# Optimization experiments

Measured on AMD Instinct MI355X. Metric: run time of the kernel, lower is better.

The kernel has to match this reference:

```python
import jax, jax.numpy as jnp
import numpy as np

N, IN_SZ, OUT_SZ = 8192, 512, 64

def setup_inputs() -> dict:
    key = jax.random.key(0)
    ks = jax.random.split(key, 7)
    s_in = 1.0 / np.sqrt(IN_SZ)
    inp = {
        "input": jax.random.normal(ks[0], (N, IN_SZ), dtype=jnp.float32),
        "Wq": jax.random.uniform(ks[1], (OUT_SZ, IN_SZ), jnp.float32, -s_in, s_in),
        "bq": jax.random.uniform(ks[2], (OUT_SZ,), jnp.float32, -s_in, s_in),
        "Wk": jax.random.uniform(ks[3], (OUT_SZ, IN_SZ), jnp.float32, -s_in, s_in),
        "bk": jax.random.uniform(ks[4], (OUT_SZ,), jnp.float32, -s_in, s_in),
        "Wv": jax.random.uniform(ks[5], (OUT_SZ, IN_SZ), jnp.float32, -s_in, s_in),
        "bv": jax.random.uniform(ks[6], (OUT_SZ,), jnp.float32, -s_in, s_in),
    }
    return inp

def reference(input, Wq, bq, Wk, bk, Wv, bv):
    # torch nn.Linear: x @ W.T + b
    q = input @ Wq.T + bq  # [N, out]
    k = input @ Wk.T + bk  # [N, out]
    v = input @ Wv.T + bv  # [N, out]
    # NOTE: original module has NO 1/sqrt(d) scaling.
    scores = jax.nn.softmax(q @ k.T, axis=-1)  # [N, N]
    return scores @ v  # [N, out]
```

## Files before the change

kernel.cpp:

```cpp
#include <hip/hip_runtime.h>
#include <math.h>

#define SA_N   8192
#define SA_IN  512
#define SA_D   64
#define G_SPL  16
#define LOG2E  1.44269504f

typedef short s16x8 __attribute__((ext_vector_type(8)));
typedef float f32x16 __attribute__((ext_vector_type(16)));

#define MFMA32(A, B, C) __builtin_amdgcn_mfma_f32_32x32x16_bf16((A), (B), (C), 0, 0, 0)

static __device__ __forceinline__ unsigned short f2bf_rn(float x) {
    unsigned int u = __float_as_uint(x);
    unsigned int r = (u + 0x7FFFu + ((u >> 16) & 1u)) >> 16;
    return (unsigned short)r;
}

static __device__ __forceinline__ void trunc_split(float f, unsigned short* hi, unsigned short* lo) {
    unsigned int u = __float_as_uint(f);
    *hi = (unsigned short)(u >> 16);
    float lf = f - __uint_as_float(u & 0xFFFF0000u);
    *lo = (unsigned short)(__float_as_uint(lf) >> 16);
}

static __device__ __forceinline__ unsigned int pack_hi16(unsigned int u0, unsigned int u1) {
    return __builtin_amdgcn_perm(u1, u0, 0x07060302u);
}

static __device__ __forceinline__ void split8(const float4 a, const float4 b, s16x8* xh, s16x8* xl) {
    union { unsigned int u[4]; s16x8 v; } H, L;
    const float f[8] = {a.x, a.y, a.z, a.w, b.x, b.y, b.z, b.w};
#pragma unroll
    for (int p = 0; p < 4; ++p) {
        const unsigned int u0 = __float_as_uint(f[2 * p]);
        const unsigned int u1 = __float_as_uint(f[2 * p + 1]);
        H.u[p] = pack_hi16(u0, u1);
        const float l0 = f[2 * p]     - __uint_as_float(u0 & 0xFFFF0000u);
        const float l1 = f[2 * p + 1] - __uint_as_float(u1 & 0xFFFF0000u);
        L.u[p] = pack_hi16(__float_as_uint(l0), __float_as_uint(l1));
    }
    *xh = H.v; *xl = L.v;
}

static __device__ __forceinline__ s16x8 pack_rn8(const float4 a, const float4 b) {
    union { unsigned int u[4]; s16x8 v; } P;
    const float f[8] = {a.x, a.y, a.z, a.w, b.x, b.y, b.z, b.w};
#pragma unroll
    for (int p = 0; p < 4; ++p)
        P.u[p] = (unsigned int)f2bf_rn(f[2 * p]) | ((unsigned int)f2bf_rn(f[2 * p + 1]) << 16);
    return P.v;
}

__global__ __launch_bounds__(256, 2) void qkv_kernel(
    const float* __restrict__ in,
    const float* __restrict__ Wq, const float* __restrict__ bq,
    const float* __restrict__ Wk, const float* __restrict__ bk,
    const float* __restrict__ Wv, const float* __restrict__ bv,
    unsigned short* __restrict__ Qhi, unsigned short* __restrict__ Qlo,
    unsigned short* __restrict__ KhiF, unsigned short* __restrict__ VF)
{
    __shared__ float cbuf[2][4][64][20];
    __shared__ __align__(16) unsigned short stage[4096];
    const int t    = threadIdx.x;
    const int w    = t >> 6;
    const int lane = t & 63;
    const int h    = lane >> 5;
    const int q32  = lane & 31;
    const int mat  = blockIdx.x >> 8;
    const int jt   = blockIdx.x & 255;
    const int rows0 = jt * 32;

    const float* W = (mat == 0) ? Wq : (mat == 1 ? Wk : Wv);
    const float* B = (mat == 0) ? bq : (mat == 1 ? bk : bv);

    f32x16 accA[2] = {};
    f32x16 accB[2] = {};

#pragma unroll 2
    for (int ksl = 0; ksl < 8; ++ksl) {
        const int ks = (w << 3) + ksl;
        const float* xp = in + (size_t)(rows0 + q32) * SA_IN + ks * 16 + h * 8;
        const float4 xa = *(const float4*)xp;
        const float4 xb = *(const float4*)(xp + 4);
        s16x8 xh, xl;
        split8(xa, xb, &xh, &xl);
#pragma unroll
        for (int mt = 0; mt < 2; ++mt) {
            const float* wp = W + (size_t)(mt * 32 + q32) * SA_IN + ks * 16 + h * 8;
            const float4 wa = *(const float4*)wp;
            const float4 wb = *(const float4*)(wp + 4);
            if (mat < 2) {
                s16x8 ah, al;
                split8(wa, wb, &ah, &al);
                accA[mt] = MFMA32(ah, xh, accA[mt]);
                accB[mt] = MFMA32(ah, xl, accB[mt]);
                accA[mt] = MFMA32(al, xh, accA[mt]);
            } else {
                const s16x8 ah = pack_rn8(wa, wb);
                accA[mt] = MFMA32(ah, xh, accA[mt]);
            }
        }
    }

#pragma unroll
    for (int mt = 0; mt < 2; ++mt) {
        f32x16 tot = accA[mt];
        if (mat < 2) {
#pragma unroll
            for (int r = 0; r < 16; ++r) tot[r] += accB[mt][r];
        }
#pragma unroll
        for (int rg = 0; rg < 4; ++rg) {
            float4 vv = { tot[4 * rg + 0], tot[4 * rg + 1],
                          tot[4 * rg + 2], tot[4 * rg + 3] };
            *(float4*)&cbuf[mt][w][lane][4 * rg] = vv;
        }
    }
    __syncthreads();
    if (w < 2) {
        const int mt = w;
        float c[16];
#pragma unroll
        for (int rg = 0; rg < 4; ++rg) {
            const float4 s0 = *(const float4*)&cbuf[mt][0][lane][4 * rg];
            const float4 s1 = *(const float4*)&cbuf[mt][1][lane][4 * rg];
            const float4 s2 = *(const float4*)&cbuf[mt][2][lane][4 * rg];
            const float4 s3 = *(const float4*)&cbuf[mt][3][lane][4 * rg];
            c[4 * rg + 0] = (s0.x + s1.x) + (s2.x + s3.x);
            c[4 * rg + 1] = (s0.y + s1.y) + (s2.y + s3.y);
            c[4 * rg + 2] = (s0.z + s1.z) + (s2.z + s3.z);
            c[4 * rg + 3] = (s0.w + s1.w) + (s2.w + s3.w);
        }
#pragma unroll
        for (int r = 0; r < 16; ++r) {
            const int o = mt * 32 + (r & 3) + 8 * (r >> 2) + 4 * h;
            float val = c[r] + B[o];
            if (mat == 0) {
                val *= LOG2E;
                unsigned short hi, lo;
                trunc_split(val, &hi, &lo);
                stage[q32 * 64 + o]        = hi;
                stage[2048 + q32 * 64 + o] = lo;
            } else if (mat == 1) {
                const int kl_ = ((o >> 4) * 64 + ((o >> 3) & 1) * 32 + q32) * 8 + (o & 7);
                stage[kl_] = f2bf_rn(val);
            } else {
                const int hp = (q32 >> 2) & 1;
                const int ip = (q32 & 3) + ((q32 >> 3) & 1) * 4;
                const int vl_ = ((o >> 5) * 2 + (q32 >> 4)) * 512
                              + hp * 256 + (o & 31) * 8 + ip;
                stage[vl_] = f2bf_rn(val);
            }
        }
    }
    __syncthreads();

    {
        const uint4* st4 = (const uint4*)stage;
        if (mat == 0) {
            for (int i = t; i < 512; i += 256) {
                unsigned short* dst = ((i < 256) ? Qhi : Qlo) + (size_t)rows0 * 64 + (i & 255) * 8;
                *(uint4*)dst = st4[i];
            }
        } else if (mat == 1) {
            if (t < 256) *(uint4*)(KhiF + (size_t)jt * 2048 + t * 8) = st4[t];
        } else {
            *(uint4*)(VF + (size_t)jt * 2048 + t * 8) = st4[t];
        }
    }
}

__global__ __launch_bounds__(512, 2) void attn_kernel(
    const unsigned short* __restrict__ Qhi, const unsigned short* __restrict__ Qlo,
    const unsigned short* __restrict__ KhiF, const unsigned short* __restrict__ VF,
    unsigned short* __restrict__ Opart, float* __restrict__ Lpart)
{
    __shared__ __align__(16) unsigned short kbuf[2][2][2048];
    const int t    = threadIdx.x;
    const int w    = t >> 6;
    const int lane = t & 63;
    const int h    = lane >> 5;
    const int q32  = lane & 31;
    const int qb   = blockIdx.x >> 4;
    const int g    = blockIdx.x & 15;
    const int q0   = (qb * 8 + w) * 32;
    const int jt0  = g * 16;

    const int half = t >> 8;
    const int ti   = t & 255;

    s16x8 qh[4], ql[4];
#pragma unroll
    for (int s = 0; s < 4; ++s) {
        const size_t off = (size_t)(q0 + q32) * 64 + s * 16 + h * 8;
        qh[s] = *reinterpret_cast<const s16x8*>(Qhi + off);
        ql[s] = *reinterpret_cast<const s16x8*>(Qlo + off);
    }

    const unsigned short* SRC = half ? VF : KhiF;

    {
        const uint4 a = *(const uint4*)(SRC + (size_t)jt0 * 2048 + ti * 8);
        *(uint4*)&kbuf[0][half][ti * 8] = a;
    }
    __syncthreads();

    f32x16 O0 = {}, O1 = {};
    float lsum = 0.f;

    for (int it = 0; it < 16; ++it) {
        const int p = it & 1;

        uint4 na;
        if (it < 15) {
            na = *(const uint4*)(SRC + (size_t)(jt0 + it + 1) * 2048 + ti * 8);
        }

        s16x8 kh[4], vv[4];
#pragma unroll
        for (int s = 0; s < 4; ++s) {
            kh[s] = *(const s16x8*)&kbuf[p][0][(s * 64 + lane) * 8];
            vv[s] = *(const s16x8*)&kbuf[p][1][(s * 64 + lane) * 8];
        }

        f32x16 Sa = {}, Sb = {};
        __builtin_amdgcn_s_setprio(1);
#pragma unroll
        for (int s = 0; s < 4; ++s) {
            Sa = MFMA32(kh[s], qh[s], Sa);
            Sb = MFMA32(kh[s], ql[s], Sb);
        }
        __builtin_amdgcn_s_setprio(0);

        float e[16];
#pragma unroll
        for (int r = 0; r < 16; ++r) e[r] = __builtin_amdgcn_exp2f(Sa[r] + Sb[r]);
        lsum += (((e[0] + e[1]) + (e[2] + e[3])) + ((e[4] + e[5]) + (e[6] + e[7])))
              + (((e[8] + e[9]) + (e[10] + e[11])) + ((e[12] + e[13]) + (e[14] + e[15])));

        union { unsigned int u[4]; s16x8 v; } P0, P1;
#pragma unroll
        for (int j2 = 0; j2 < 4; ++j2) {
            P0.u[j2] = pack_hi16(__float_as_uint(e[2 * j2]),     __float_as_uint(e[2 * j2 + 1]));
            P1.u[j2] = pack_hi16(__float_as_uint(e[8 + 2 * j2]), __float_as_uint(e[8 + 2 * j2 + 1]));
        }

        __builtin_amdgcn_s_setprio(1);
        O0 = MFMA32(vv[0], P0.v, O0);
        O0 = MFMA32(vv[1], P1.v, O0);
        O1 = MFMA32(vv[2], P0.v, O1);
        O1 = MFMA32(vv[3], P1.v, O1);
        __builtin_amdgcn_s_setprio(0);

        if (it < 15) {
            *(uint4*)&kbuf[1 - p][half][ti * 8] = na;
        }
        __syncthreads();
    }

    lsum += __shfl_xor(lsum, 32, 64);

    const size_t qg = (size_t)g * SA_N + q0 + q32;
#pragma unroll
    for (int rg = 0; rg < 4; ++rg) {
        const int d0 = 8 * rg + 4 * h;
        uint2 s0, s1;
        s0.x = (unsigned int)f2bf_rn(O0[4 * rg + 0]) | ((unsigned int)f2bf_rn(O0[4 * rg + 1]) << 16);
        s0.y = (unsigned int)f2bf_rn(O0[4 * rg + 2]) | ((unsigned int)f2bf_rn(O0[4 * rg + 3]) << 16);
        s1.x = (unsigned int)f2bf_rn(O1[4 * rg + 0]) | ((unsigned int)f2bf_rn(O1[4 * rg + 1]) << 16);
        s1.y = (unsigned int)f2bf_rn(O1[4 * rg + 2]) | ((unsigned int)f2bf_rn(O1[4 * rg + 3]) << 16);
        *(uint2*)(Opart + qg * 64 + d0)      = s0;
        *(uint2*)(Opart + qg * 64 + d0 + 32) = s1;
    }
    if (h == 0) Lpart[qg] = lsum;
}

__global__ __launch_bounds__(256) void combine_kernel(
    const unsigned short* __restrict__ Opart, const float* __restrict__ Lpart,
    float* __restrict__ out)
{
    const int tid = blockIdx.x * 256 + threadIdx.x;
    const int q  = tid >> 5;
    const int dp = tid & 31;
    const unsigned int* OP = (const unsigned int*)Opart;
    float s0 = 0.f, s1 = 0.f, lt = 0.f;
#pragma unroll
    for (int g = 0; g < G_SPL; ++g) {
        const unsigned int v = OP[((size_t)g * SA_N + q) * 32 + dp];
        s0 += __uint_as_float(v << 16);
        s1 += __uint_as_float(v & 0xFFFF0000u);
        lt += Lpart[(size_t)g * SA_N + q];
    }
    float2 r = { s0 / lt, s1 / lt };
    *(float2*)&out[(size_t)q * 64 + dp * 2] = r;
}

extern "C" void kernel_launch(void* const* d_in, const int* in_sizes, int n_in,
                              void* d_out, int out_size, void* d_ws, size_t ws_size,
                              hipStream_t stream) {
    const float* input = (const float*)d_in[0];
    const float* Wq    = (const float*)d_in[1];
    const float* bq    = (const float*)d_in[2];
    const float* Wk    = (const float*)d_in[3];
    const float* bk    = (const float*)d_in[4];
    const float* Wv    = (const float*)d_in[5];
    const float* bv    = (const float*)d_in[6];
    float* out = (float*)d_out;

    const size_t SEG = (size_t)SA_N * 64;
    unsigned short* Qhi  = (unsigned short*)d_ws;
    unsigned short* Qlo  = Qhi  + SEG;
    unsigned short* KhiF = Qlo  + SEG;
    unsigned short* VF   = KhiF + SEG;
    unsigned short* Opart = VF  + SEG;
    float*          Lpart = (float*)(Opart + (size_t)G_SPL * SA_N * 64);

    qkv_kernel<<<768, 256, 0, stream>>>(input, Wq, bq, Wk, bk, Wv, bv,
                                        Qhi, Qlo, KhiF, VF);
    attn_kernel<<<32 * G_SPL, 512, 0, stream>>>(Qhi, Qlo, KhiF, VF, Opart, Lpart);
    combine_kernel<<<1024, 256, 0, stream>>>(Opart, Lpart, out);
}
```

Before: 126.2 us.

## Process two 32-row query tiles per wave to reuse K/V tiles

Each wave now handles 64 query rows (two 32-row tiles) instead of 32, so every K/V tile staged in shared memory is reused for twice as many queries. The grid is halved to 256 blocks and launch bounds drop to one block per SIMD slot to make room for the extra accumulators and Q registers. This cuts K/V global loads and LDS reads per query. The cost is higher register pressure, fewer blocks than CUs on a 256-CU part, and less latency hiding.

```diff
diff --git a/kernel.cpp b/kernel.cpp
--- a/kernel.cpp
+++ b/kernel.cpp
@@ -172,7 +172,7 @@
     }
 }
 
-__global__ __launch_bounds__(512, 2) void attn_kernel(
+__global__ __launch_bounds__(512, 1) void attn_kernel(
     const unsigned short* __restrict__ Qhi, const unsigned short* __restrict__ Qlo,
     const unsigned short* __restrict__ KhiF, const unsigned short* __restrict__ VF,
     unsigned short* __restrict__ Opart, float* __restrict__ Lpart)
@@ -185,18 +185,21 @@
     const int q32  = lane & 31;
     const int qb   = blockIdx.x >> 4;
     const int g    = blockIdx.x & 15;
-    const int q0   = (qb * 8 + w) * 32;
+    const int q0   = qb * 512 + w * 64;
     const int jt0  = g * 16;
 
     const int half = t >> 8;
     const int ti   = t & 255;
 
-    s16x8 qh[4], ql[4];
+    s16x8 qh0[4], ql0[4], qh1[4], ql1[4];
 #pragma unroll
     for (int s = 0; s < 4; ++s) {
-        const size_t off = (size_t)(q0 + q32) * 64 + s * 16 + h * 8;
-        qh[s] = *reinterpret_cast<const s16x8*>(Qhi + off);
-        ql[s] = *reinterpret_cast<const s16x8*>(Qlo + off);
+        const size_t off0 = (size_t)(q0 + q32) * 64 + s * 16 + h * 8;
+        const size_t off1 = (size_t)(q0 + 32 + q32) * 64 + s * 16 + h * 8;
+        qh0[s] = *reinterpret_cast<const s16x8*>(Qhi + off0);
+        ql0[s] = *reinterpret_cast<const s16x8*>(Qlo + off0);
+        qh1[s] = *reinterpret_cast<const s16x8*>(Qhi + off1);
+        ql1[s] = *reinterpret_cast<const s16x8*>(Qlo + off1);
     }
 
     const unsigned short* SRC = half ? VF : KhiF;
@@ -207,8 +210,8 @@
     }
     __syncthreads();
 
-    f32x16 O0 = {}, O1 = {};
-    float lsum = 0.f;
+    f32x16 O00 = {}, O01 = {}, O10 = {}, O11 = {};
+    float ls0 = 0.f, ls1 = 0.f;
 
     for (int it = 0; it < 16; ++it) {
         const int p = it & 1;
@@ -225,34 +228,67 @@
             vv[s] = *(const s16x8*)&kbuf[p][1][(s * 64 + lane) * 8];
         }
 
-        f32x16 Sa = {}, Sb = {};
-        __builtin_amdgcn_s_setprio(1);
-#pragma unroll
-        for (int s = 0; s < 4; ++s) {
-            Sa = MFMA32(kh[s], qh[s], Sa);
-            Sb = MFMA32(kh[s], ql[s], Sb);
-        }
-        __builtin_amdgcn_s_setprio(0);
-
-        float e[16];
-#pragma unroll
-        for (int r = 0; r < 16; ++r) e[r] = __builtin_amdgcn_exp2f(Sa[r] + Sb[r]);
-        lsum += (((e[0] + e[1]) + (e[2] + e[3])) + ((e[4] + e[5]) + (e[6] + e[7])))
-              + (((e[8] + e[9]) + (e[10] + e[11])) + ((e[12] + e[13]) + (e[14] + e[15])));
-
-        union { unsigned int u[4]; s16x8 v; } P0, P1;
-#pragma unroll
-        for (int j2 = 0; j2 < 4; ++j2) {
-            P0.u[j2] = pack_hi16(__float_as_uint(e[2 * j2]),     __float_as_uint(e[2 * j2 + 1]));
-            P1.u[j2] = pack_hi16(__float_as_uint(e[8 + 2 * j2]), __float_as_uint(e[8 + 2 * j2 + 1]));
-        }
-
-        __builtin_amdgcn_s_setprio(1);
-        O0 = MFMA32(vv[0], P0.v, O0);
-        O0 = MFMA32(vv[1], P1.v, O0);
-        O1 = MFMA32(vv[2], P0.v, O1);
-        O1 = MFMA32(vv[3], P1.v, O1);
-        __builtin_amdgcn_s_setprio(0);
+        {
+            f32x16 Sa = {}, Sb = {};
+            __builtin_amdgcn_s_setprio(1);
+#pragma unroll
+            for (int s = 0; s < 4; ++s) {
+                Sa = MFMA32(kh[s], qh0[s], Sa);
+                Sb = MFMA32(kh[s], ql0[s], Sb);
+            }
+            __builtin_amdgcn_s_setprio(0);
+
+            float e[16];
+#pragma unroll
+            for (int r = 0; r < 16; ++r) e[r] = __builtin_amdgcn_exp2f(Sa[r] + Sb[r]);
+            ls0 += (((e[0] + e[1]) + (e[2] + e[3])) + ((e[4] + e[5]) + (e[6] + e[7])))
+                 + (((e[8] + e[9]) + (e[10] + e[11])) + ((e[12] + e[13]) + (e[14] + e[15])));
+
+            union { unsigned int u[4]; s16x8 v; } P0, P1;
+#pragma unroll
+            for (int j2 = 0; j2 < 4; ++j2) {
+                P0.u[j2] = pack_hi16(__float_as_uint(e[2 * j2]),     __float_as_uint(e[2 * j2 + 1]));
+                P1.u[j2] = pack_hi16(__float_as_uint(e[8 + 2 * j2]), __float_as_uint(e[8 + 2 * j2 + 1]));
+            }
+
+            __builtin_amdgcn_s_setprio(1);
+            O00 = MFMA32(vv[0], P0.v, O00);
+            O00 = MFMA32(vv[1], P1.v, O00);
+            O01 = MFMA32(vv[2], P0.v, O01);
+            O01 = MFMA32(vv[3], P1.v, O01);
+            __builtin_amdgcn_s_setprio(0);
+        }
+
+        {
+            f32x16 Sa = {}, Sb = {};
+            __builtin_amdgcn_s_setprio(1);
+#pragma unroll
+            for (int s = 0; s < 4; ++s) {
+                Sa = MFMA32(kh[s], qh1[s], Sa);
+                Sb = MFMA32(kh[s], ql1[s], Sb);
+            }
+            __builtin_amdgcn_s_setprio(0);
+
+            float e[16];
+#pragma unroll
+            for (int r = 0; r < 16; ++r) e[r] = __builtin_amdgcn_exp2f(Sa[r] + Sb[r]);
+            ls1 += (((e[0] + e[1]) + (e[2] + e[3])) + ((e[4] + e[5]) + (e[6] + e[7])))
+                 + (((e[8] + e[9]) + (e[10] + e[11])) + ((e[12] + e[13]) + (e[14] + e[15])));
+
+            union { unsigned int u[4]; s16x8 v; } P0, P1;
+#pragma unroll
+            for (int j2 = 0; j2 < 4; ++j2) {
+                P0.u[j2] = pack_hi16(__float_as_uint(e[2 * j2]),     __float_as_uint(e[2 * j2 + 1]));
+                P1.u[j2] = pack_hi16(__float_as_uint(e[8 + 2 * j2]), __float_as_uint(e[8 + 2 * j2 + 1]));
+            }
+
+            __builtin_amdgcn_s_setprio(1);
+            O10 = MFMA32(vv[0], P0.v, O10);
+            O10 = MFMA32(vv[1], P1.v, O10);
+            O11 = MFMA32(vv[2], P0.v, O11);
+            O11 = MFMA32(vv[3], P1.v, O11);
+            __builtin_amdgcn_s_setprio(0);
+        }
 
         if (it < 15) {
             *(uint4*)&kbuf[1 - p][half][ti * 8] = na;
@@ -260,21 +296,33 @@
         __syncthreads();
     }
 
-    lsum += __shfl_xor(lsum, 32, 64);
-
-    const size_t qg = (size_t)g * SA_N + q0 + q32;
+    ls0 += __shfl_xor(ls0, 32, 64);
+    ls1 += __shfl_xor(ls1, 32, 64);
+
+    const size_t qg0 = (size_t)g * SA_N + q0 + q32;
+    const size_t qg1 = qg0 + 32;
 #pragma unroll
     for (int rg = 0; rg < 4; ++rg) {
         const int d0 = 8 * rg + 4 * h;
         uint2 s0, s1;
-        s0.x = (unsigned int)f2bf_rn(O0[4 * rg + 0]) | ((unsigned int)f2bf_rn(O0[4 * rg + 1]) << 16);
-        s0.y = (unsigned int)f2bf_rn(O0[4 * rg + 2]) | ((unsigned int)f2bf_rn(O0[4 * rg + 3]) << 16);
-        s1.x = (unsigned int)f2bf_rn(O1[4 * rg + 0]) | ((unsigned int)f2bf_rn(O1[4 * rg + 1]) << 16);
-        s1.y = (unsigned int)f2bf_rn(O1[4 * rg + 2]) | ((unsigned int)f2bf_rn(O1[4 * rg + 3]) << 16);
-        *(uint2*)(Opart + qg * 64 + d0)      = s0;
-        *(uint2*)(Opart + qg * 64 + d0 + 32) = s1;
-    }
-    if (h == 0) Lpart[qg] = lsum;
+        s0.x = (unsigned int)f2bf_rn(O00[4 * rg + 0]) | ((unsigned int)f2bf_rn(O00[4 * rg + 1]) << 16);
+        s0.y = (unsigned int)f2bf_rn(O00[4 * rg + 2]) | ((unsigned int)f2bf_rn(O00[4 * rg + 3]) << 16);
+        s1.x = (unsigned int)f2bf_rn(O01[4 * rg + 0]) | ((unsigned int)f2bf_rn(O01[4 * rg + 1]) << 16);
+        s1.y = (unsigned int)f2bf_rn(O01[4 * rg + 2]) | ((unsigned int)f2bf_rn(O01[4 * rg + 3]) << 16);
+        *(uint2*)(Opart + qg0 * 64 + d0)      = s0;
+        *(uint2*)(Opart + qg0 * 64 + d0 + 32) = s1;
+        uint2 t0, t1;
+        t0.x = (unsigned int)f2bf_rn(O10[4 * rg + 0]) | ((unsigned int)f2bf_rn(O10[4 * rg + 1]) << 16);
+        t0.y = (unsigned int)f2bf_rn(O10[4 * rg + 2]) | ((unsigned int)f2bf_rn(O10[4 * rg + 3]) << 16);
+        t1.x = (unsigned int)f2bf_rn(O11[4 * rg + 0]) | ((unsigned int)f2bf_rn(O11[4 * rg + 1]) << 16);
+        t1.y = (unsigned int)f2bf_rn(O11[4 * rg + 2]) | ((unsigned int)f2bf_rn(O11[4 * rg + 3]) << 16);
+        *(uint2*)(Opart + qg1 * 64 + d0)      = t0;
+        *(uint2*)(Opart + qg1 * 64 + d0 + 32) = t1;
+    }
+    if (h == 0) {
+        Lpart[qg0] = ls0;
+        Lpart[qg1] = ls1;
+    }
 }
 
 __global__ __launch_bounds__(256) void combine_kernel(
@@ -319,6 +367,6 @@
 
     qkv_kernel<<<768, 256, 0, stream>>>(input, Wq, bq, Wk, bk, Wv, bv,
                                         Qhi, Qlo, KhiF, VF);
-    attn_kernel<<<32 * G_SPL, 512, 0, stream>>>(Qhi, Qlo, KhiF, VF, Opart, Lpart);
+    attn_kernel<<<16 * G_SPL, 512, 0, stream>>>(Qhi, Qlo, KhiF, VF, Opart, Lpart);
     combine_kernel<<<1024, 256, 0, stream>>>(Opart, Lpart, out);
 }
```

After: 126.7 us. No clear change (+0.4%).
